# Performance work log

Measured on AMD Instinct MI355X. Metric: run time of the kernel, lower is better.

## Reference

```python
import jax, jax.numpy as jnp
import numpy as np

NL, D, H = 12, 768, 12   # layers, d_model, heads (Clinical-Longformer config)
DH = D // H
FF = 4 * D
VOCAB = 50265
MAXPOS = 4098
W = 256                   # one-sided sliding window (attention_window=512 -> 256 per side)
EPS = 1e-5

def layer_norm(x, g, b):
    m = jnp.mean(x, axis=-1, keepdims=True)
    v = jnp.mean(jnp.square(x - m), axis=-1, keepdims=True)
    return (x - m) * jax.lax.rsqrt(v + EPS) * g + b

def sliding_window_attention(q, k, v, key_mask):
    # q,k,v: [B,H,S,dh]; key_mask: [B,S] float (1=keep). S must be a multiple of W.
    # Chunked banded attention: query chunk c attends to key chunks c-1,c,c+1,
    # then an exact |i-j| <= W band mask is applied (HF Longformer local attention).
    B, Hh, S, dh = q.shape
    nc = S // W
    kp = jnp.pad(k, ((0, 0), (0, 0), (W, W), (0, 0))).reshape(B, Hh, nc + 2, W, dh)
    vp = jnp.pad(v, ((0, 0), (0, 0), (W, W), (0, 0))).reshape(B, Hh, nc + 2, W, dh)
    kc = jnp.concatenate([kp[:, :, :-2], kp[:, :, 1:-1], kp[:, :, 2:]], axis=3)  # [B,H,nc,3W,dh]
    vc = jnp.concatenate([vp[:, :, :-2], vp[:, :, 1:-1], vp[:, :, 2:]], axis=3)
    mp = jnp.pad(key_mask, ((0, 0), (W, W))).reshape(B, nc + 2, W)
    mc = jnp.concatenate([mp[:, :-2], mp[:, 1:-1], mp[:, 2:]], axis=2)            # [B,nc,3W]
    qc = q.reshape(B, Hh, nc, W, dh)
    scores = jnp.einsum('bhcqd,bhckd->bhcqk', qc, kc) * (1.0 / np.sqrt(dh))      # [B,H,nc,W,3W]
    qi = jnp.arange(W)[:, None]
    kj = jnp.arange(3 * W)[None, :]
    band = (kj >= qi) & (kj <= qi + 2 * W)        # exact |i-j| <= W band within the 3-chunk window
    valid = band[None, None, None] & (mc[:, None, :, None, :] > 0)
    attn = jax.nn.softmax(jnp.where(valid, scores, -1e9), axis=-1)
    return jnp.einsum('bhcqk,bhckd->bhcqd', attn, vc).reshape(B, Hh, S, dh)

def encoder(input_ids, attention_mask, word_emb, pos_emb, type_emb, emb_g, emb_b, layer_params):
    B, S = input_ids.shape
    mask = attention_mask.astype(jnp.float32)
    # RoBERTa-style position ids with padding_idx=1
    pos_ids = jnp.cumsum(attention_mask, axis=1) * attention_mask + 1
    h = word_emb[input_ids] + pos_emb[pos_ids] + type_emb[0]
    h = layer_norm(h, emb_g, emb_b)

    def step(h, p):
        Wq, bq, Wk, bk, Wv, bv, Wo, bo, g1, b1, W1, c1, W2, c2, g2, b2 = p
        q = (h @ Wq + bq).reshape(B, S, H, DH).transpose(0, 2, 1, 3)
        k = (h @ Wk + bk).reshape(B, S, H, DH).transpose(0, 2, 1, 3)
        v = (h @ Wv + bv).reshape(B, S, H, DH).transpose(0, 2, 1, 3)
        a = sliding_window_attention(q, k, v, mask)
        o = a.transpose(0, 2, 1, 3).reshape(B, S, D) @ Wo + bo
        h = layer_norm(h + o, g1, b1)
        f = jax.nn.gelu(h @ W1 + c1, approximate=False) @ W2 + c2
        h = layer_norm(h + f, g2, b2)
        return h, None

    h, _ = jax.lax.scan(step, h, layer_params)
    return h[:, 0, :]   # report_feat = last_hidden_state[:, 0, :]

def setup_inputs():
    key = jax.random.key(0)
    ks = iter(jax.random.split(key, 16))
    s = 0.02
    B, S = 1, 2048
    def w(shape):
        return s * jax.random.normal(next(ks), shape, jnp.float32)
    inp = {}
    inp['input_ids'] = jax.random.randint(next(ks), (B, S), 0, VOCAB, dtype=jnp.int32)
    inp['attention_mask'] = jnp.ones((B, S), dtype=jnp.int32)
    inp['word_emb'] = w((VOCAB, D))
    inp['pos_emb'] = w((MAXPOS, D))
    inp['type_emb'] = w((2, D))
    inp['emb_g'] = jnp.ones((D,), jnp.float32)
    inp['emb_b'] = jnp.zeros((D,), jnp.float32)
    inp['Wq'] = w((NL, D, D)); inp['bq'] = jnp.zeros((NL, D), jnp.float32)
    inp['Wk'] = w((NL, D, D)); inp['bk'] = jnp.zeros((NL, D), jnp.float32)
    inp['Wv'] = w((NL, D, D)); inp['bv'] = jnp.zeros((NL, D), jnp.float32)
    inp['Wo'] = w((NL, D, D)); inp['bo'] = jnp.zeros((NL, D), jnp.float32)
    inp['g1'] = jnp.ones((NL, D), jnp.float32); inp['b1'] = jnp.zeros((NL, D), jnp.float32)
    inp['W1'] = w((NL, D, FF)); inp['c1'] = jnp.zeros((NL, FF), jnp.float32)
    inp['W2'] = w((NL, FF, D)); inp['c2'] = jnp.zeros((NL, D), jnp.float32)
    inp['g2'] = jnp.ones((NL, D), jnp.float32); inp['b2'] = jnp.zeros((NL, D), jnp.float32)
    return inp

def reference(input_ids, attention_mask, word_emb, pos_emb, type_emb, emb_g, emb_b,
              Wq, bq, Wk, bk, Wv, bv, Wo, bo, g1, b1, W1, c1, W2, c2, g2, b2):
    lp = (Wq, bq, Wk, bk, Wv, bv, Wo, bo, g1, b1, W1, c1, W2, c2, g2, b2)
    return encoder(input_ids, attention_mask, word_emb, pos_emb, type_emb, emb_g, emb_b, lp)
```

## Files before the change

kernel.cpp:

```cpp
#include <hip/hip_runtime.h>
#include <hip/hip_bf16.h>
#include <cmath>

#define S_LEN 2048
#define DM 768
#define NH 12
#define DHEAD 64
#define FF_DIM 3072
#define NLAYERS 12
#define WIN 256

typedef __attribute__((ext_vector_type(4))) float f32x4;
typedef __attribute__((ext_vector_type(8))) short s16x8;
typedef __attribute__((ext_vector_type(4))) short s16x4;
typedef __attribute__((ext_vector_type(4))) float fragc;

#define OFF_QKVT 0L
#define OFF_WOT  1769472L
#define OFF_W1T  2359296L
#define OFF_W2T  4718592L
#define WSLAB    7077888L

__device__ __forceinline__ float bf2f(ushort u) {
  union { unsigned u; float f; } v; v.u = ((unsigned)u) << 16; return v.f;
}
__device__ __forceinline__ ushort f2bf(float f) {
  union { float f; unsigned u; } v; v.f = f;
  unsigned r = v.u + 0x7fffu + ((v.u >> 16) & 1u);
  return (ushort)(r >> 16);
}

typedef __attribute__((address_space(1))) const void GVp;
typedef __attribute__((address_space(3))) void LVp;
__device__ __forceinline__ void gload16(const void* g, void* l) {
  __builtin_amdgcn_global_load_lds((GVp*)g, (LVp*)l, 16, 0, 0);
}

template<int EPI, int BM, int BN, bool SPLIT>
__global__ __launch_bounds__(256) void gemm_t(
    const ushort* __restrict__ A0, int lda,
    const ushort* __restrict__ B0, int ldb,
    void* __restrict__ C0, void* __restrict__ C1, int ldc,
    const float* __restrict__ bias0,
    const float* __restrict__ res0,
    int Kdim)
{
  constexpr int MF = BM / 32;
  constexpr int NF = BN / 32;
  constexpr int MT = S_LEN / BM;
  __shared__ ushort As[2][BM * 64];
  __shared__ ushort Bs[2][BN * 64];

  const int tid  = threadIdx.x;
  const int lane = tid & 63;
  const int wave = tid >> 6;
  const int z    = SPLIT ? blockIdx.z : 0;
  const int koff = z * Kdim;

  const int nwg = gridDim.x;
  const int o   = blockIdx.x;
  const int id2 = (o & 7) * (nwg >> 3) + (o >> 3);
  const int mt  = id2 % MT;
  const int nt  = id2 / MT;

  const long aoff = (long)mt * BM * lda;
  const long boff = (long)nt * BN * ldb;
  const long coff = (long)mt * BM * ldc + (long)nt * BN;
  const float* bias = bias0 ? bias0 + nt * BN : nullptr;

  fragc acc[MF][NF] = {};
  const int l15 = lane & 15;
  const int g   = lane >> 4;
  const int rx  = l15 & 7;
  const int MR0 = (wave & 1) * (BM / 2);
  const int NC0 = (wave >> 1) * (BN / 2);
  const int srow = lane >> 3;
  const int scol = ((lane & 7) ^ srow) * 8;

  auto stage = [&](int buf, int k0) {
    #pragma unroll
    for (int j = 0; j < BM / 32; j++) {
      int c = wave * (BM / 32) + j;
      gload16(A0 + aoff + (long)(c * 8 + srow) * lda + k0 + scol,
              (char*)&As[buf][0] + c * 1024);
    }
    #pragma unroll
    for (int j = 0; j < BN / 32; j++) {
      int c = wave * (BN / 32) + j;
      gload16(B0 + boff + (long)(c * 8 + srow) * ldb + k0 + scol,
              (char*)&Bs[buf][0] + c * 1024);
    }
  };

  stage(0, koff);
  __syncthreads();
  int cur = 0;
  for (int k0 = koff; k0 < koff + Kdim; k0 += 64) {
    if (k0 + 64 < koff + Kdim) stage(cur ^ 1, k0 + 64);
    s16x8 afr[MF][2], bfr[NF][2];
    #pragma unroll
    for (int ks = 0; ks < 2; ks++) {
      #pragma unroll
      for (int mi = 0; mi < MF; mi++)
        afr[mi][ks] = *(const s16x8*)((const char*)&As[cur][0] +
                      (MR0 + mi * 16 + l15) * 128 + (((ks * 4 + g) ^ rx) << 4));
      #pragma unroll
      for (int ni = 0; ni < NF; ni++)
        bfr[ni][ks] = *(const s16x8*)((const char*)&Bs[cur][0] +
                      (NC0 + ni * 16 + l15) * 128 + (((ks * 4 + g) ^ rx) << 4));
    }
    #pragma unroll
    for (int ks = 0; ks < 2; ks++)
      #pragma unroll
      for (int mi = 0; mi < MF; mi++)
        #pragma unroll
        for (int ni = 0; ni < NF; ni++)
          acc[mi][ni] = __builtin_amdgcn_mfma_f32_16x16x32_bf16(afr[mi][ks], bfr[ni][ks], acc[mi][ni], 0, 0, 0);
    __syncthreads();
    cur ^= 1;
  }

  float*  Cf = (float*)(z == 0 ? C0 : C1);
  ushort* Cb = (ushort*)C0;
  const int rb = g * 4;
  #pragma unroll
  for (int mi = 0; mi < MF; mi++)
  #pragma unroll
  for (int ni = 0; ni < NF; ni++)
  #pragma unroll
  for (int r = 0; r < 4; r++) {
    int row = MR0 + mi * 16 + rb + r;
    int col = NC0 + ni * 16 + l15;
    long ci = coff + (long)row * ldc + col;
    float v = acc[mi][ni][r];
    if (EPI == 0) {
      if (bias) v += bias[col];
      Cb[ci] = f2bf(v);
    } else if (EPI == 2) {
      v += bias[col];
      v = 0.5f * v * (1.0f + erff(v * 0.70710678118654752f));
      Cb[ci] = f2bf(v);
    } else {
      if (z == 0) v += bias[col] + res0[ci];
      Cf[ci] = v;
    }
  }
}

__global__ __launch_bounds__(256) void attn_k(
    const ushort* __restrict__ qkvb,
    const ushort* __restrict__ vbT,
    const int*    __restrict__ am,
    ushort*       __restrict__ aob)
{
  __shared__ ushort Qs[64 * 64];
  __shared__ ushort Ks[128 * 64];
  __shared__ ushort Vs[64 * 128];
  __shared__ ushort Ps[4][16 * 128];
  __shared__ float  ambias[768];

  const int tid  = threadIdx.x;
  const int lane = tid & 63;
  const int w    = tid >> 6;
  const int l15  = lane & 15;
  const int g    = lane >> 4;
  const int h    = blockIdx.y;
  const int q0   = blockIdx.x * 64;
  const int korigin = (q0 >> 8) * 256 - WIN;
  const int q    = q0 + w * 16 + l15;

  #pragma unroll
  for (int j = 0; j < 2; j++) {
    int c = w * 2 + j;
    int stored = c * 1024 + lane * 16;
    int row = stored >> 7;
    int within = (stored & 127) ^ ((row & 7) << 4);
    gload16(qkvb + (size_t)(q0 + row) * 2304 + h * DHEAD + (within >> 1),
            (char*)Qs + stored);
  }
  for (int j = tid; j < 768; j += 256) {
    int tok = korigin + j;
    bool ok = (tok >= 0) && (tok < S_LEN) && (am[tok] != 0);
    ambias[j] = ok ? 0.0f : -1e30f;
  }

  f32x4 ot[4] = {};
  float m = -1e20f, l = 0.0f;

  const int lo = q0 - WIN < 0 ? 0 : q0 - WIN;
  const int hi = (q0 + 63 + WIN > S_LEN - 1) ? S_LEN - 1 : q0 + 63 + WIN;

  for (int kt = 0; kt < 6; kt++) {
    const int tok0 = korigin + kt * 128;
    if (tok0 + 127 < lo || tok0 > hi) continue;

    #pragma unroll
    for (int j = 0; j < 4; j++) {
      int c = w * 4 + j;
      int stored = c * 1024 + lane * 16;
      int row = stored >> 7;
      int within = (stored & 127) ^ ((row & 7) << 4);
      int tok = tok0 + row;
      tok = tok < 0 ? 0 : (tok > S_LEN - 1 ? S_LEN - 1 : tok);
      gload16(qkvb + (size_t)tok * 2304 + DM + h * DHEAD + (within >> 1),
              (char*)Ks + stored);
    }
    #pragma unroll
    for (int j = 0; j < 4; j++) {
      int c = w * 4 + j;
      int stored = c * 1024 + lane * 16;
      int row = stored >> 8;
      int within = (stored & 255) ^ ((row & 7) << 4);
      int tok = tok0 + (within >> 1);
      tok = tok < 0 ? 0 : (tok > S_LEN - 8 ? S_LEN - 8 : tok);
      gload16(vbT + ((size_t)h * DHEAD + row) * S_LEN + tok,
              (char*)Vs + stored);
    }
    __syncthreads();

    s16x8 qf[2];
    #pragma unroll
    for (int ks = 0; ks < 2; ks++)
      qf[ks] = *(const s16x8*)((const char*)Qs + (w * 16 + l15) * 128 +
                               (((g * 16 + ks * 64)) ^ ((l15 & 7) << 4)));

    f32x4 st[8] = {};
    #pragma unroll
    for (int ks = 0; ks < 2; ks++) {
      #pragma unroll
      for (int mi = 0; mi < 8; mi++) {
        int row = mi * 16 + l15;
        s16x8 af = *(const s16x8*)((const char*)Ks + row * 128 +
                                   ((g * 16 + ks * 64) ^ ((row & 7) << 4)));
        st[mi] = __builtin_amdgcn_mfma_f32_16x16x32_bf16(af, qf[ks], st[mi], 0, 0, 0);
      }
    }

    float mx = -1e30f;
    float sv[8][4];
    #pragma unroll
    for (int mi = 0; mi < 8; mi++)
      #pragma unroll
      for (int r = 0; r < 4; r++) {
        int kw  = kt * 128 + mi * 16 + g * 4 + r;
        int tok = korigin + kw;
        float s = st[mi][r] * 0.125f + ambias[kw];
        bool band = (tok >= q - WIN) && (tok <= q + WIN);
        s = band ? s : -1e30f;
        sv[mi][r] = s;
        mx = fmaxf(mx, s);
      }
    mx = fmaxf(mx, __shfl_xor(mx, 16));
    mx = fmaxf(mx, __shfl_xor(mx, 32));

    float m_new = fmaxf(fmaxf(m, mx), -1e20f);
    float sf = __expf(m - m_new);
    float rs = 0.0f;
    #pragma unroll
    for (int mi = 0; mi < 8; mi++) {
      s16x4 pk;
      #pragma unroll
      for (int r = 0; r < 4; r++) {
        float p = __expf(sv[mi][r] - m_new);
        rs += p;
        pk[r] = (short)f2bf(p);
      }
      *(s16x4*)((char*)&Ps[w][0] + l15 * 256 + ((mi * 32 + g * 8) ^ ((l15 & 7) << 4))) = pk;
    }
    rs += __shfl_xor(rs, 16);
    rs += __shfl_xor(rs, 32);
    l = l * sf + rs;
    m = m_new;
    #pragma unroll
    for (int mi = 0; mi < 4; mi++)
      #pragma unroll
      for (int r = 0; r < 4; r++) ot[mi][r] *= sf;

    #pragma unroll
    for (int ks = 0; ks < 4; ks++) {
      s16x8 pf = *(const s16x8*)((const char*)&Ps[w][0] + l15 * 256 +
                                 ((ks * 64 + g * 16) ^ ((l15 & 7) << 4)));
      #pragma unroll
      for (int mi = 0; mi < 4; mi++) {
        int row = mi * 16 + l15;
        s16x8 vf = *(const s16x8*)((const char*)Vs + row * 256 +
                                   ((ks * 64 + g * 16) ^ ((row & 7) << 4)));
        ot[mi] = __builtin_amdgcn_mfma_f32_16x16x32_bf16(vf, pf, ot[mi], 0, 0, 0);
      }
    }
    __syncthreads();
  }

  float inv = l > 0.0f ? 1.0f / l : 0.0f;
  #pragma unroll
  for (int mi = 0; mi < 4; mi++) {
    s16x4 o;
    #pragma unroll
    for (int r = 0; r < 4; r++) o[r] = (short)f2bf(ot[mi][r] * inv);
    *(s16x4*)(aob + (size_t)q * DM + h * DHEAD + mi * 16 + g * 4) = o;
  }
}

__global__ __launch_bounds__(256) void cvtT_k(const float* __restrict__ src, ushort* __restrict__ dst,
                                              int N, int K, long sstride, long dstride, int dnoff)
{
  __shared__ float tile[32][33];
  const int tid = threadIdx.x;
  src += (long)blockIdx.z * sstride;
  dst += (long)blockIdx.z * dstride;
  int n0 = blockIdx.x * 32, k0 = blockIdx.y * 32;
  #pragma unroll
  for (int j = 0; j < 4; j++) {
    int r = j * 8 + (tid >> 5);
    int c = tid & 31;
    tile[r][c] = src[(long)(k0 + r) * N + n0 + c];
  }
  __syncthreads();
  #pragma unroll
  for (int j = 0; j < 4; j++) {
    int n = j * 8 + (tid >> 5);
    int k = tid & 31;
    dst[(long)(dnoff + n0 + n) * K + k0 + k] = f2bf(tile[k][n]);
  }
}

__global__ __launch_bounds__(256) void transv_k(const ushort* __restrict__ qkvb, ushort* __restrict__ vbT)
{
  __shared__ ushort tile[64][72];
  const int tid = threadIdx.x;
  const int h = blockIdx.y;
  const int t0 = blockIdx.x * 64;
  #pragma unroll
  for (int it = 0; it < 4; it++) {
    int r = it * 16 + (tid >> 4);
    int c = (tid & 15) * 4;
    *(s16x4*)&tile[r][c] = *(const s16x4*)&qkvb[(long)(t0 + r) * 2304 + 2 * DM + h * DHEAD + c];
  }
  __syncthreads();
  #pragma unroll
  for (int it = 0; it < 4; it++) {
    int d = it * 16 + (tid >> 4);
    int t = (tid & 15) * 4;
    s16x4 v;
    #pragma unroll
    for (int j = 0; j < 4; j++) v[j] = (short)tile[t + j][d];
    *(s16x4*)&vbT[((long)h * DHEAD + d) * S_LEN + t0 + t] = v;
  }
}

__global__ void biascat_k(const float* __restrict__ bq, const float* __restrict__ bk,
                          const float* __restrict__ bv, float* __restrict__ out)
{
  int i = blockIdx.x * 256 + threadIdx.x;
  if (i >= NLAYERS * 3 * DM) return;
  int l = i / (3 * DM), j = i % (3 * DM);
  const float* src = j < DM ? bq : (j < 2 * DM ? bk : bv);
  out[(long)l * 3 * DM + j] = src[(long)l * DM + (j % DM)];
}

__global__ __launch_bounds__(256) void ln2_k(const float* __restrict__ X, float* __restrict__ Y,
                                             ushort* __restrict__ Yb,
                                             const float* __restrict__ g, const float* __restrict__ b)
{
  int row  = (int)((blockIdx.x * blockDim.x + threadIdx.x) >> 6);
  int lane = threadIdx.x & 63;
  const float* x = X + (long)row * DM;
  float v[12]; float sum = 0.f;
  #pragma unroll
  for (int i = 0; i < 12; i++) { v[i] = x[i * 64 + lane]; sum += v[i]; }
  #pragma unroll
  for (int off = 32; off; off >>= 1) sum += __shfl_xor(sum, off);
  float mean = sum * (1.0f / 768.0f);
  float var = 0.f;
  #pragma unroll
  for (int i = 0; i < 12; i++) { float d = v[i] - mean; var += d * d; }
  #pragma unroll
  for (int off = 32; off; off >>= 1) var += __shfl_xor(var, off);
  float rstd = rsqrtf(var * (1.0f / 768.0f) + 1e-5f);
  #pragma unroll
  for (int i = 0; i < 12; i++) {
    int c = i * 64 + lane;
    float y = (v[i] - mean) * rstd * g[c] + b[c];
    Y[(long)row * DM + c] = y;
    Yb[(long)row * DM + c] = f2bf(y);
  }
}

__global__ __launch_bounds__(256) void ln2d_k(const float* __restrict__ X, const float* __restrict__ X2,
                                              float* __restrict__ Y, ushort* __restrict__ Yb,
                                              const float* __restrict__ g, const float* __restrict__ b)
{
  int row  = (int)((blockIdx.x * blockDim.x + threadIdx.x) >> 6);
  int lane = threadIdx.x & 63;
  const float* x  = X  + (long)row * DM;
  const float* x2 = X2 + (long)row * DM;
  float v[12]; float sum = 0.f;
  #pragma unroll
  for (int i = 0; i < 12; i++) { v[i] = x[i * 64 + lane] + x2[i * 64 + lane]; sum += v[i]; }
  #pragma unroll
  for (int off = 32; off; off >>= 1) sum += __shfl_xor(sum, off);
  float mean = sum * (1.0f / 768.0f);
  float var = 0.f;
  #pragma unroll
  for (int i = 0; i < 12; i++) { float d = v[i] - mean; var += d * d; }
  #pragma unroll
  for (int off = 32; off; off >>= 1) var += __shfl_xor(var, off);
  float rstd = rsqrtf(var * (1.0f / 768.0f) + 1e-5f);
  #pragma unroll
  for (int i = 0; i < 12; i++) {
    int c = i * 64 + lane;
    float y = (v[i] - mean) * rstd * g[c] + b[c];
    Y[(long)row * DM + c] = y;
    Yb[(long)row * DM + c] = f2bf(y);
  }
}

__global__ void scan_k(const int* __restrict__ am, int* __restrict__ pos)
{
  __shared__ int buf[S_LEN];
  int t = threadIdx.x;
  buf[t] = am[t]; buf[t + 1024] = am[t + 1024];
  __syncthreads();
  for (int off = 1; off < S_LEN; off <<= 1) {
    int a0 = buf[t];
    int a1 = buf[t + 1024];
    int b0 = (t >= off) ? buf[t - off] : 0;
    int b1 = (t + 1024 >= off) ? buf[t + 1024 - off] : 0;
    __syncthreads();
    buf[t] = a0 + b0; buf[t + 1024] = a1 + b1;
    __syncthreads();
  }
  pos[t]        = buf[t] * am[t] + 1;
  pos[t + 1024] = buf[t + 1024] * am[t + 1024] + 1;
}

__global__ __launch_bounds__(256) void embed_k(const int* __restrict__ ids, const int* __restrict__ pos,
    const float* __restrict__ we, const float* __restrict__ pe, const float* __restrict__ te,
    float* __restrict__ out)
{
  int s = blockIdx.x / 3;
  int d = (blockIdx.x % 3) * 256 + threadIdx.x;
  out[(long)s * DM + d] = we[(long)ids[s] * DM + d] + pe[(long)pos[s] * DM + d] + te[d];
}

__global__ void out_k(const float* __restrict__ h, float* __restrict__ out)
{
  int i = blockIdx.x * 256 + threadIdx.x;
  if (i < DM) out[i] = h[i];
}

extern "C" void kernel_launch(void* const* d_in, const int* in_sizes, int n_in,
                              void* d_out, int out_size, void* d_ws, size_t ws_size,
                              hipStream_t stream)
{
  const int*   ids = (const int*)d_in[0];
  const int*   am  = (const int*)d_in[1];
  const float* we  = (const float*)d_in[2];
  const float* pe  = (const float*)d_in[3];
  const float* te  = (const float*)d_in[4];
  const float* eg  = (const float*)d_in[5];
  const float* eb  = (const float*)d_in[6];
  const float* Wq  = (const float*)d_in[7];
  const float* bq  = (const float*)d_in[8];
  const float* Wk  = (const float*)d_in[9];
  const float* bk  = (const float*)d_in[10];
  const float* Wv  = (const float*)d_in[11];
  const float* bv  = (const float*)d_in[12];
  const float* Wo  = (const float*)d_in[13];
  const float* bo  = (const float*)d_in[14];
  const float* g1  = (const float*)d_in[15];
  const float* b1  = (const float*)d_in[16];
  const float* W1  = (const float*)d_in[17];
  const float* c1  = (const float*)d_in[18];
  const float* W2  = (const float*)d_in[19];
  const float* c2  = (const float*)d_in[20];
  const float* g2  = (const float*)d_in[21];
  const float* b2  = (const float*)d_in[22];

  char* w = (char*)d_ws;
  float*  h    = (float*)w;  w += (size_t)S_LEN * DM * 4;
  float*  tmp  = (float*)w;  w += (size_t)S_LEN * DM * 4;
  float*  tmp2 = (float*)w;  w += (size_t)S_LEN * DM * 4;
  ushort* hb   = (ushort*)w; w += (size_t)S_LEN * DM * 2;
  ushort* qkvb = (ushort*)w; w += (size_t)S_LEN * 3 * DM * 2;
  ushort* vbT  = (ushort*)w; w += (size_t)NH * DHEAD * S_LEN * 2;
  ushort* aob  = (ushort*)w; w += (size_t)S_LEN * DM * 2;
  ushort* ffnb = (ushort*)w; w += (size_t)S_LEN * FF_DIM * 2;
  ushort* wT   = (ushort*)w; w += (size_t)NLAYERS * WSLAB * 2;
  float*  bqkv = (float*)w;  w += (size_t)NLAYERS * 3 * DM * 4;
  int*    pos  = (int*)w;

  scan_k<<<1, 1024, 0, stream>>>(am, pos);
  embed_k<<<dim3(S_LEN * 3), 256, 0, stream>>>(ids, pos, we, pe, te, tmp);
  ln2_k<<<dim3(S_LEN / 4), 256, 0, stream>>>(tmp, h, hb, eg, eb);
  biascat_k<<<dim3((NLAYERS * 3 * DM + 255) / 256), 256, 0, stream>>>(bq, bk, bv, bqkv);
  cvtT_k<<<dim3(24, 24, NLAYERS), 256, 0, stream>>>(Wq, wT + OFF_QKVT, DM, DM, (long)DM*DM, WSLAB, 0);
  cvtT_k<<<dim3(24, 24, NLAYERS), 256, 0, stream>>>(Wk, wT + OFF_QKVT, DM, DM, (long)DM*DM, WSLAB, DM);
  cvtT_k<<<dim3(24, 24, NLAYERS), 256, 0, stream>>>(Wv, wT + OFF_QKVT, DM, DM, (long)DM*DM, WSLAB, 2*DM);
  cvtT_k<<<dim3(24, 24, NLAYERS), 256, 0, stream>>>(Wo, wT + OFF_WOT, DM, DM, (long)DM*DM, WSLAB, 0);
  cvtT_k<<<dim3(96, 24, NLAYERS), 256, 0, stream>>>(W1, wT + OFF_W1T, FF_DIM, DM, (long)DM*FF_DIM, WSLAB, 0);
  cvtT_k<<<dim3(24, 96, NLAYERS), 256, 0, stream>>>(W2, wT + OFF_W2T, DM, FF_DIM, (long)DM*FF_DIM, WSLAB, 0);

  for (int L = 0; L < NLAYERS; L++) {
    const ushort* wTL = wT + (size_t)L * WSLAB;

    gemm_t<0,64,128,false><<<dim3(576), 256, 0, stream>>>(
        hb, DM, wTL + OFF_QKVT, DM, qkvb, nullptr, 3 * DM,
        bqkv + (size_t)L * 3 * DM, nullptr, DM);
    transv_k<<<dim3(S_LEN / 64, NH), 256, 0, stream>>>(qkvb, vbT);

    attn_k<<<dim3(S_LEN / 64, NH), 256, 0, stream>>>(qkvb, vbT, am, aob);

    gemm_t<3,64,64,true><<<dim3(384, 1, 2), 256, 0, stream>>>(
        aob, DM, wTL + OFF_WOT, DM, tmp, tmp2, DM,
        bo + (size_t)L * DM, h, 384);
    ln2d_k<<<dim3(S_LEN / 4), 256, 0, stream>>>(tmp, tmp2, h, hb,
        g1 + (size_t)L * DM, b1 + (size_t)L * DM);

    gemm_t<2,64,128,false><<<dim3(768), 256, 0, stream>>>(
        hb, DM, wTL + OFF_W1T, DM, ffnb, nullptr, FF_DIM,
        c1 + (size_t)L * FF_DIM, nullptr, DM);
    gemm_t<3,64,64,true><<<dim3(384, 1, 2), 256, 0, stream>>>(
        ffnb, FF_DIM, wTL + OFF_W2T, FF_DIM, tmp, tmp2, DM,
        c2 + (size_t)L * DM, h, 1536);
    ln2d_k<<<dim3(S_LEN / 4), 256, 0, stream>>>(tmp, tmp2, h, hb,
        g2 + (size_t)L * DM, b2 + (size_t)L * DM);
  }

  out_k<<<3, 256, 0, stream>>>(h, (float*)d_out);
}
```

Before: 1.513 ms.

## Double-buffer attention K tiles, store split-K partials in bf16, vectorize layernorm

The attention kernel now double-buffers K tiles and prefetches the next V tile so global loads overlap compute. It also iterates only over the needed key tiles and remaps its 1D grid across heads. MFMA sections in both GEMM and attention get raised wave priority via s_setprio. The split-K GEMM epilogue writes bf16 partials instead of fp32, and the layernorm kernels use vectorized contiguous loads and stores. Storing the residual-plus-partial sums in bf16 cuts memory traffic but loses precision in the residual path.

New measurement: 1.486 ms. Within noise of the previous version (-1.8%).

```diff
diff --git a/kernel.cpp b/kernel.cpp
--- a/kernel.cpp
+++ b/kernel.cpp
@@ -109,6 +109,7 @@
         bfr[ni][ks] = *(const s16x8*)((const char*)&Bs[cur][0] +
                       (NC0 + ni * 16 + l15) * 128 + (((ks * 4 + g) ^ rx) << 4));
     }
+    __builtin_amdgcn_s_setprio(1);
     #pragma unroll
     for (int ks = 0; ks < 2; ks++)
       #pragma unroll
@@ -116,12 +117,13 @@
         #pragma unroll
         for (int ni = 0; ni < NF; ni++)
           acc[mi][ni] = __builtin_amdgcn_mfma_f32_16x16x32_bf16(afr[mi][ks], bfr[ni][ks], acc[mi][ni], 0, 0, 0);
+    __builtin_amdgcn_s_setprio(0);
     __syncthreads();
     cur ^= 1;
   }
 
-  float*  Cf = (float*)(z == 0 ? C0 : C1);
-  ushort* Cb = (ushort*)C0;
+  ushort* Cb  = (ushort*)C0;
+  ushort* Cb1 = (ushort*)(z == 0 ? C0 : C1);
   const int rb = g * 4;
   #pragma unroll
   for (int mi = 0; mi < MF; mi++)
@@ -142,7 +144,7 @@
       Cb[ci] = f2bf(v);
     } else {
       if (z == 0) v += bias[col] + res0[ci];
-      Cf[ci] = v;
+      Cb1[ci] = f2bf(v);
     }
   }
 }
@@ -154,7 +156,7 @@
     ushort*       __restrict__ aob)
 {
   __shared__ ushort Qs[64 * 64];
-  __shared__ ushort Ks[128 * 64];
+  __shared__ ushort Ks[2][128 * 64];
   __shared__ ushort Vs[64 * 128];
   __shared__ ushort Ps[4][16 * 128];
   __shared__ float  ambias[768];
@@ -164,36 +166,15 @@
   const int w    = tid >> 6;
   const int l15  = lane & 15;
   const int g    = lane >> 4;
-  const int h    = blockIdx.y;
-  const int q0   = blockIdx.x * 64;
+  const int o    = blockIdx.x;
+  const int id2  = (o & 7) * 48 + (o >> 3);
+  const int h    = id2 >> 5;
+  const int q0   = (id2 & 31) * 64;
   const int korigin = (q0 >> 8) * 256 - WIN;
   const int q    = q0 + w * 16 + l15;
 
-  #pragma unroll
-  for (int j = 0; j < 2; j++) {
-    int c = w * 2 + j;
-    int stored = c * 1024 + lane * 16;
-    int row = stored >> 7;
-    int within = (stored & 127) ^ ((row & 7) << 4);
-    gload16(qkvb + (size_t)(q0 + row) * 2304 + h * DHEAD + (within >> 1),
-            (char*)Qs + stored);
-  }
-  for (int j = tid; j < 768; j += 256) {
-    int tok = korigin + j;
-    bool ok = (tok >= 0) && (tok < S_LEN) && (am[tok] != 0);
-    ambias[j] = ok ? 0.0f : -1e30f;
-  }
-
-  f32x4 ot[4] = {};
-  float m = -1e20f, l = 0.0f;
-
-  const int lo = q0 - WIN < 0 ? 0 : q0 - WIN;
-  const int hi = (q0 + 63 + WIN > S_LEN - 1) ? S_LEN - 1 : q0 + 63 + WIN;
-
-  for (int kt = 0; kt < 6; kt++) {
-    const int tok0 = korigin + kt * 128;
-    if (tok0 + 127 < lo || tok0 > hi) continue;
-
+  auto stageK = [&](int buf, int kt) {
+    int tok0 = korigin + kt * 128;
     #pragma unroll
     for (int j = 0; j < 4; j++) {
       int c = w * 4 + j;
@@ -203,8 +184,11 @@
       int tok = tok0 + row;
       tok = tok < 0 ? 0 : (tok > S_LEN - 1 ? S_LEN - 1 : tok);
       gload16(qkvb + (size_t)tok * 2304 + DM + h * DHEAD + (within >> 1),
-              (char*)Ks + stored);
-    }
+              (char*)&Ks[buf][0] + stored);
+    }
+  };
+  auto stageV = [&](int kt) {
+    int tok0 = korigin + kt * 128;
     #pragma unroll
     for (int j = 0; j < 4; j++) {
       int c = w * 4 + j;
@@ -216,25 +200,58 @@
       gload16(vbT + ((size_t)h * DHEAD + row) * S_LEN + tok,
               (char*)Vs + stored);
     }
-    __syncthreads();
-
-    s16x8 qf[2];
-    #pragma unroll
-    for (int ks = 0; ks < 2; ks++)
-      qf[ks] = *(const s16x8*)((const char*)Qs + (w * 16 + l15) * 128 +
-                               (((g * 16 + ks * 64)) ^ ((l15 & 7) << 4)));
+  };
+
+  #pragma unroll
+  for (int j = 0; j < 2; j++) {
+    int c = w * 2 + j;
+    int stored = c * 1024 + lane * 16;
+    int row = stored >> 7;
+    int within = (stored & 127) ^ ((row & 7) << 4);
+    gload16(qkvb + (size_t)(q0 + row) * 2304 + h * DHEAD + (within >> 1),
+            (char*)Qs + stored);
+  }
+  for (int j = tid; j < 768; j += 256) {
+    int tok = korigin + j;
+    bool ok = (tok >= 0) && (tok < S_LEN) && (am[tok] != 0);
+    ambias[j] = ok ? 0.0f : -1e30f;
+  }
+
+  const int lo = q0 - WIN < 0 ? 0 : q0 - WIN;
+  const int hi = (q0 + 63 + WIN > S_LEN - 1) ? S_LEN - 1 : q0 + 63 + WIN;
+  const int kt_start = (lo - korigin) >> 7;
+  const int kt_end   = (hi - korigin) >> 7;
+
+  stageK(0, kt_start);
+  stageV(kt_start);
+  __syncthreads();
+
+  s16x8 qf[2];
+  #pragma unroll
+  for (int ks = 0; ks < 2; ks++)
+    qf[ks] = *(const s16x8*)((const char*)Qs + (w * 16 + l15) * 128 +
+                             ((g * 16 + ks * 64) ^ ((l15 & 7) << 4)));
+
+  f32x4 ot[4] = {};
+  float m = -1e20f, l = 0.0f;
+  int cur = 0;
+
+  for (int kt = kt_start; kt <= kt_end; kt++) {
+    if (kt < kt_end) stageK(cur ^ 1, kt + 1);
 
     f32x4 st[8] = {};
+    __builtin_amdgcn_s_setprio(1);
     #pragma unroll
     for (int ks = 0; ks < 2; ks++) {
       #pragma unroll
       for (int mi = 0; mi < 8; mi++) {
         int row = mi * 16 + l15;
-        s16x8 af = *(const s16x8*)((const char*)Ks + row * 128 +
+        s16x8 af = *(const s16x8*)((const char*)&Ks[cur][0] + row * 128 +
                                    ((g * 16 + ks * 64) ^ ((row & 7) << 4)));
         st[mi] = __builtin_amdgcn_mfma_f32_16x16x32_bf16(af, qf[ks], st[mi], 0, 0, 0);
       }
     }
+    __builtin_amdgcn_s_setprio(0);
 
     float mx = -1e30f;
     float sv[8][4];
@@ -276,6 +293,9 @@
       #pragma unroll
       for (int r = 0; r < 4; r++) ot[mi][r] *= sf;
 
+    __syncthreads();
+
+    __builtin_amdgcn_s_setprio(1);
     #pragma unroll
     for (int ks = 0; ks < 4; ks++) {
       s16x8 pf = *(const s16x8*)((const char*)&Ps[w][0] + l15 * 256 +
@@ -288,16 +308,20 @@
         ot[mi] = __builtin_amdgcn_mfma_f32_16x16x32_bf16(vf, pf, ot[mi], 0, 0, 0);
       }
     }
+    __builtin_amdgcn_s_setprio(0);
     __syncthreads();
+
+    if (kt < kt_end) stageV(kt + 1);
+    cur ^= 1;
   }
 
   float inv = l > 0.0f ? 1.0f / l : 0.0f;
   #pragma unroll
   for (int mi = 0; mi < 4; mi++) {
-    s16x4 o;
-    #pragma unroll
-    for (int r = 0; r < 4; r++) o[r] = (short)f2bf(ot[mi][r] * inv);
-    *(s16x4*)(aob + (size_t)q * DM + h * DHEAD + mi * 16 + g * 4) = o;
+    s16x4 oo;
+    #pragma unroll
+    for (int r = 0; r < 4; r++) oo[r] = (short)f2bf(ot[mi][r] * inv);
+    *(s16x4*)(aob + (size_t)q * DM + h * DHEAD + mi * 16 + g * 4) = oo;
   }
 }
 
@@ -364,10 +388,14 @@
 {
   int row  = (int)((blockIdx.x * blockDim.x + threadIdx.x) >> 6);
   int lane = threadIdx.x & 63;
-  const float* x = X + (long)row * DM;
+  const float* x = X + (long)row * DM + lane * 12;
   float v[12]; float sum = 0.f;
   #pragma unroll
-  for (int i = 0; i < 12; i++) { v[i] = x[i * 64 + lane]; sum += v[i]; }
+  for (int j = 0; j < 3; j++) {
+    f32x4 t = *(const f32x4*)(x + j * 4);
+    #pragma unroll
+    for (int r = 0; r < 4; r++) { v[j * 4 + r] = t[r]; sum += t[r]; }
+  }
   #pragma unroll
   for (int off = 32; off; off >>= 1) sum += __shfl_xor(sum, off);
   float mean = sum * (1.0f / 768.0f);
@@ -377,26 +405,44 @@
   #pragma unroll
   for (int off = 32; off; off >>= 1) var += __shfl_xor(var, off);
   float rstd = rsqrtf(var * (1.0f / 768.0f) + 1e-5f);
-  #pragma unroll
-  for (int i = 0; i < 12; i++) {
-    int c = i * 64 + lane;
-    float y = (v[i] - mean) * rstd * g[c] + b[c];
-    Y[(long)row * DM + c] = y;
-    Yb[(long)row * DM + c] = f2bf(y);
-  }
-}
-
-__global__ __launch_bounds__(256) void ln2d_k(const float* __restrict__ X, const float* __restrict__ X2,
-                                              float* __restrict__ Y, ushort* __restrict__ Yb,
-                                              const float* __restrict__ g, const float* __restrict__ b)
+  float* y = Y + (long)row * DM + lane * 12;
+  ushort* yb = Yb + (long)row * DM + lane * 12;
+  const float* gg = g + lane * 12;
+  const float* bb = b + lane * 12;
+  #pragma unroll
+  for (int j = 0; j < 3; j++) {
+    f32x4 go = *(const f32x4*)(gg + j * 4);
+    f32x4 bo = *(const f32x4*)(bb + j * 4);
+    f32x4 yo; s16x4 yh;
+    #pragma unroll
+    for (int r = 0; r < 4; r++) {
+      float t = (v[j * 4 + r] - mean) * rstd * go[r] + bo[r];
+      yo[r] = t; yh[r] = (short)f2bf(t);
+    }
+    *(f32x4*)(y + j * 4) = yo;
+    *(s16x4*)(yb + j * 4) = yh;
+  }
+}
+
+__global__ __launch_bounds__(256) void ln2db_k(const ushort* __restrict__ X0, const ushort* __restrict__ X1,
+                                               float* __restrict__ Y, ushort* __restrict__ Yb,
+                                               const float* __restrict__ g, const float* __restrict__ b)
 {
   int row  = (int)((blockIdx.x * blockDim.x + threadIdx.x) >> 6);
   int lane = threadIdx.x & 63;
-  const float* x  = X  + (long)row * DM;
-  const float* x2 = X2 + (long)row * DM;
+  const ushort* x0 = X0 + (long)row * DM + lane * 12;
+  const ushort* x1 = X1 + (long)row * DM + lane * 12;
   float v[12]; float sum = 0.f;
   #pragma unroll
-  for (int i = 0; i < 12; i++) { v[i] = x[i * 64 + lane] + x2[i * 64 + lane]; sum += v[i]; }
+  for (int j = 0; j < 3; j++) {
+    s16x4 a = *(const s16x4*)(x0 + j * 4);
+    s16x4 c = *(const s16x4*)(x1 + j * 4);
+    #pragma unroll
+    for (int r = 0; r < 4; r++) {
+      float t = bf2f((ushort)a[r]) + bf2f((ushort)c[r]);
+      v[j * 4 + r] = t; sum += t;
+    }
+  }
   #pragma unroll
   for (int off = 32; off; off >>= 1) sum += __shfl_xor(sum, off);
   float mean = sum * (1.0f / 768.0f);
@@ -406,12 +452,22 @@
   #pragma unroll
   for (int off = 32; off; off >>= 1) var += __shfl_xor(var, off);
   float rstd = rsqrtf(var * (1.0f / 768.0f) + 1e-5f);
-  #pragma unroll
-  for (int i = 0; i < 12; i++) {
-    int c = i * 64 + lane;
-    float y = (v[i] - mean) * rstd * g[c] + b[c];
-    Y[(long)row * DM + c] = y;
-    Yb[(long)row * DM + c] = f2bf(y);
+  float* y = Y + (long)row * DM + lane * 12;
+  ushort* yb = Yb + (long)row * DM + lane * 12;
+  const float* gg = g + lane * 12;
+  const float* bb = b + lane * 12;
+  #pragma unroll
+  for (int j = 0; j < 3; j++) {
+    f32x4 go = *(const f32x4*)(gg + j * 4);
+    f32x4 bo = *(const f32x4*)(bb + j * 4);
+    f32x4 yo; s16x4 yh;
+    #pragma unroll
+    for (int r = 0; r < 4; r++) {
+      float t = (v[j * 4 + r] - mean) * rstd * go[r] + bo[r];
+      yo[r] = t; yh[r] = (short)f2bf(t);
+    }
+    *(f32x4*)(y + j * 4) = yo;
+    *(s16x4*)(yb + j * 4) = yh;
   }
 }
 
@@ -490,6 +546,9 @@
   float*  bqkv = (float*)w;  w += (size_t)NLAYERS * 3 * DM * 4;
   int*    pos  = (int*)w;
 
+  ushort* tb0 = (ushort*)tmp;
+  ushort* tb1 = (ushort*)tmp2;
+
   scan_k<<<1, 1024, 0, stream>>>(am, pos);
   embed_k<<<dim3(S_LEN * 3), 256, 0, stream>>>(ids, pos, we, pe, te, tmp);
   ln2_k<<<dim3(S_LEN / 4), 256, 0, stream>>>(tmp, h, hb, eg, eb);
@@ -509,21 +568,21 @@
         bqkv + (size_t)L * 3 * DM, nullptr, DM);
     transv_k<<<dim3(S_LEN / 64, NH), 256, 0, stream>>>(qkvb, vbT);
 
-    attn_k<<<dim3(S_LEN / 64, NH), 256, 0, stream>>>(qkvb, vbT, am, aob);
+    attn_k<<<dim3(384), 256, 0, stream>>>(qkvb, vbT, am, aob);
 
     gemm_t<3,64,64,true><<<dim3(384, 1, 2), 256, 0, stream>>>(
-        aob, DM, wTL + OFF_WOT, DM, tmp, tmp2, DM,
+        aob, DM, wTL + OFF_WOT, DM, tb0, tb1, DM,
         bo + (size_t)L * DM, h, 384);
-    ln2d_k<<<dim3(S_LEN / 4), 256, 0, stream>>>(tmp, tmp2, h, hb,
+    ln2db_k<<<dim3(S_LEN / 4), 256, 0, stream>>>(tb0, tb1, h, hb,
         g1 + (size_t)L * DM, b1 + (size_t)L * DM);
 
     gemm_t<2,64,128,false><<<dim3(768), 256, 0, stream>>>(
         hb, DM, wTL + OFF_W1T, DM, ffnb, nullptr, FF_DIM,
         c1 + (size_t)L * FF_DIM, nullptr, DM);
     gemm_t<3,64,64,true><<<dim3(384, 1, 2), 256, 0, stream>>>(
-        ffnb, FF_DIM, wTL + OFF_W2T, FF_DIM, tmp, tmp2, DM,
+        ffnb, FF_DIM, wTL + OFF_W2T, FF_DIM, tb0, tb1, DM,
         c2 + (size_t)L * DM, h, 1536);
-    ln2d_k<<<dim3(S_LEN / 4), 256, 0, stream>>>(tmp, tmp2, h, hb,
+    ln2db_k<<<dim3(S_LEN / 4), 256, 0, stream>>>(tb0, tb1, h, hb,
         g2 + (size_t)L * DM, b2 + (size_t)L * DM);
   }
 
```
